# Kernel tuning notes

Hardware: AMD Instinct MI355X
Metric: run time of the kernel (lower is better)

Reference implementation:

```python
import jax, jax.numpy as jnp
import numpy as np

N_NODES = 100000
N_EDGES = 1600000
NEG_SLOPE = 0.2
EPS = 1e-16


def _gat_layer(x, src, dst, W, att_src, att_dst, bias, heads, out_ch):
    # x: [N, F_in]; src/dst: [E'] (self-loops already appended)
    n = x.shape[0]
    h = (x @ W).reshape(n, heads, out_ch)                      # [N, H, C]
    a_src = (h * att_src[None]).sum(-1)                        # [N, H]
    a_dst = (h * att_dst[None]).sum(-1)                        # [N, H]
    e = a_src[src] + a_dst[dst]                                # [E', H]
    e = jnp.where(e > 0, e, NEG_SLOPE * e)                     # leaky_relu
    # segment softmax over incoming edges of each dst node
    m = jax.ops.segment_max(e, dst, num_segments=n)            # [N, H]
    ex = jnp.exp(e - m[dst])                                   # [E', H]
    s = jax.ops.segment_sum(ex, dst, num_segments=n)           # [N, H]
    alpha = ex / (s[dst] + EPS)                                # [E', H]
    msg = h[src] * alpha[:, :, None]                           # [E', H, C]
    out = jax.ops.segment_sum(msg, dst, num_segments=n)        # [N, H, C]
    return out.reshape(n, heads * out_ch) + bias


def setup_inputs() -> dict:
    key = jax.random.key(0)
    ks = jax.random.split(key, 10)
    x = jax.random.normal(ks[0], (N_NODES, 165), dtype=jnp.float32)
    src = jax.random.randint(ks[1], (N_EDGES,), 0, N_NODES, dtype=jnp.int32)
    dst = jax.random.randint(ks[2], (N_EDGES,), 0, N_NODES, dtype=jnp.int32)
    glorot = lambda k, shp: jax.random.normal(k, shp, dtype=jnp.float32) * jnp.sqrt(2.0 / (shp[0] + shp[-1]))
    W1 = glorot(ks[3], (165, 256))
    att_src1 = glorot(ks[4], (4, 64))
    att_dst1 = glorot(ks[5], (4, 64))
    b1 = jnp.zeros((256,), dtype=jnp.float32)
    W2 = glorot(ks[6], (256, 2))
    att_src2 = glorot(ks[7], (1, 2))
    att_dst2 = glorot(ks[8], (1, 2))
    b2 = jnp.zeros((2,), dtype=jnp.float32)
    return {"x": x, "src": src, "dst": dst,
            "W1": W1, "att_src1": att_src1, "att_dst1": att_dst1, "b1": b1,
            "W2": W2, "att_src2": att_src2, "att_dst2": att_dst2, "b2": b2}


def reference(x, src, dst, W1, att_src1, att_dst1, b1, W2, att_src2, att_dst2, b2):
    n = x.shape[0]
    # PyG GATConv adds self-loops by default
    loops = jnp.arange(n, dtype=src.dtype)
    s = jnp.concatenate([src, loops])
    d = jnp.concatenate([dst, loops])
    h = _gat_layer(x, s, d, W1, att_src1, att_dst1, b1, heads=4, out_ch=64)
    h = jax.nn.relu(h)
    # F.dropout with training=False is identity (eval mode)
    out = _gat_layer(h, s, d, W2, att_src2, att_dst2, b2, heads=1, out_ch=2)
    return jax.nn.log_softmax(out, axis=1)
```

## Files before the change

### kernel.cpp

```cpp
#include <hip/hip_runtime.h>
#include <math.h>

#define NN 100000
#define NE 1600000
#define ET (NE + NN)
#define NEG 0.2f
#define KP 192
#define GEMM_BLKS (NN / 32)
#define SLOTS 64

typedef __attribute__((ext_vector_type(8))) short short8;
typedef __attribute__((ext_vector_type(4))) float floatx4;

__device__ __forceinline__ unsigned short f2bf(float f) {
    unsigned u = __float_as_uint(f);
    unsigned r = u + 0x7fffu + ((u >> 16) & 1u);
    return (unsigned short)(r >> 16);
}
__device__ __forceinline__ float bflo(unsigned x) { return __uint_as_float(x << 16); }
__device__ __forceinline__ float bfhi(unsigned x) { return __uint_as_float(x & 0xFFFF0000u); }

__global__ __launch_bounds__(256) void k_prep(const float* __restrict__ W,
                                              const float* __restrict__ x,
                                              unsigned short* __restrict__ Wt,
                                              int* __restrict__ deg,
                                              unsigned* __restrict__ xbf32) {
    const int gid = blockIdx.x * 256 + threadIdx.x;
    const int G = gridDim.x * 256;
    for (int idx = gid; idx < 256 * KP; idx += G) {
        const int n = idx / KP, k = idx - n * KP;
        Wt[idx] = (k < 165) ? f2bf(W[k * 256 + n]) : (unsigned short)0;
    }
    for (int i = gid; i < NN; i += G) deg[i] = 0;
    for (int p = gid; p < NN * (KP / 2); p += G) {
        const int n = p / (KP / 2), i = p - n * (KP / 2);
        const int k0 = 2 * i;
        const float v0 = (k0 < 165) ? x[(size_t)n * 165 + k0] : 0.0f;
        const float v1 = (k0 + 1 < 165) ? x[(size_t)n * 165 + k0 + 1] : 0.0f;
        xbf32[p] = (unsigned)f2bf(v0) | ((unsigned)f2bf(v1) << 16);
    }
}

__global__ __launch_bounds__(256) void k_histscat(const int* __restrict__ src,
                                                  const int* __restrict__ dst,
                                                  int* __restrict__ deg,
                                                  int* __restrict__ esrc) {
    const int e = blockIdx.x * 256 + threadIdx.x;
    if (e >= ET) return;
    int s, d;
    if (e < NE) { s = src[e]; d = dst[e]; } else { s = d = e - NE; }
    const int r = atomicAdd(&deg[d], 1);
    if (r < SLOTS) esrc[(d << 6) + r] = s;
}

__global__ __launch_bounds__(256) void k_gemm1(const unsigned short* __restrict__ xbf,
                                               const unsigned short* __restrict__ Wt,
                                               const float* __restrict__ att_s,
                                               const float* __restrict__ att_d,
                                               unsigned short* __restrict__ h1,
                                               float* __restrict__ a_src,
                                               float* __restrict__ a_dst) {
    __shared__ __align__(16) unsigned lds_p[32 * 132];
    const int t = threadIdx.x;
    const int n0 = blockIdx.x * 32;
    const int lane = t & 63, hd = t >> 6;
    const int r16 = lane & 15, quad = lane >> 4;
    floatx4 zero4 = {0.0f, 0.0f, 0.0f, 0.0f};
    floatx4 acc[2][4];
#pragma unroll
    for (int mm = 0; mm < 2; ++mm)
#pragma unroll
        for (int nn = 0; nn < 4; ++nn) acc[mm][nn] = zero4;

    const unsigned short* xr0 = xbf + (size_t)(n0 + r16) * KP;
    const unsigned short* xr1 = xbf + (size_t)(n0 + 16 + r16) * KP;
#pragma unroll
    for (int ks = 0; ks < 6; ++ks) {
        const int kb = ks * 32 + quad * 8;
        short8 a0 = *(const short8*)(xr0 + kb);
        short8 a1 = *(const short8*)(xr1 + kb);
        short8 bf[4];
#pragma unroll
        for (int nn = 0; nn < 4; ++nn)
            bf[nn] = *(const short8*)(Wt + (size_t)(hd * 64 + nn * 16 + r16) * KP + kb);
#pragma unroll
        for (int nn = 0; nn < 4; ++nn) {
            acc[0][nn] = __builtin_amdgcn_mfma_f32_16x16x32_bf16(a0, bf[nn], acc[0][nn], 0, 0, 0);
            acc[1][nn] = __builtin_amdgcn_mfma_f32_16x16x32_bf16(a1, bf[nn], acc[1][nn], 0, 0, 0);
        }
    }

    float asw[4], adw[4];
#pragma unroll
    for (int nn = 0; nn < 4; ++nn) {
        asw[nn] = att_s[hd * 64 + nn * 16 + r16];
        adw[nn] = att_d[hd * 64 + nn * 16 + r16];
    }
#pragma unroll
    for (int mm = 0; mm < 2; ++mm)
#pragma unroll
        for (int r = 0; r < 4; ++r) {
            float ps = acc[mm][0][r] * asw[0] + acc[mm][1][r] * asw[1] +
                       acc[mm][2][r] * asw[2] + acc[mm][3][r] * asw[3];
            float pd = acc[mm][0][r] * adw[0] + acc[mm][1][r] * adw[1] +
                       acc[mm][2][r] * adw[2] + acc[mm][3][r] * adw[3];
            ps += __shfl_xor(ps, 1); ps += __shfl_xor(ps, 2);
            ps += __shfl_xor(ps, 4); ps += __shfl_xor(ps, 8);
            pd += __shfl_xor(pd, 1); pd += __shfl_xor(pd, 2);
            pd += __shfl_xor(pd, 4); pd += __shfl_xor(pd, 8);
            if (r16 == 0) {
                const int node = n0 + mm * 16 + quad * 4 + r;
                a_src[node * 4 + hd] = ps;
                a_dst[node * 4 + hd] = pd;
            }
        }

#pragma unroll
    for (int mm = 0; mm < 2; ++mm)
#pragma unroll
        for (int nn = 0; nn < 4; ++nn)
#pragma unroll
            for (int r = 0; r < 4; ++r) {
                const float v = acc[mm][nn][r];
                const float o = __shfl_xor(v, 1);
                if ((lane & 1) == 0) {
                    const unsigned pk = (unsigned)f2bf(v) | ((unsigned)f2bf(o) << 16);
                    lds_p[(mm * 16 + quad * 4 + r) * 132 + hd * 32 + nn * 8 + (r16 >> 1)] = pk;
                }
            }
    __syncthreads();
    {
        const int row = t & 31, seg = t >> 5;
        const unsigned* p = &lds_p[row * 132 + seg * 16];
        uint4 d0 = *(const uint4*)(p);
        uint4 d1 = *(const uint4*)(p + 4);
        uint4 d2 = *(const uint4*)(p + 8);
        uint4 d3 = *(const uint4*)(p + 12);
        unsigned short* hp = h1 + (size_t)(n0 + row) * 256 + seg * 32;
        *(uint4*)(hp) = d0;
        *(uint4*)(hp + 8) = d1;
        *(uint4*)(hp + 16) = d2;
        *(uint4*)(hp + 24) = d3;
    }
}

__global__ __launch_bounds__(256) void k_l1agg(const unsigned short* __restrict__ h1,
                                               const float* __restrict__ a_src,
                                               const float* __restrict__ a_dst,
                                               const int* __restrict__ deg,
                                               const int* __restrict__ esrc,
                                               const float* __restrict__ b1,
                                               const float* __restrict__ W2,
                                               const float* __restrict__ att_s2,
                                               const float* __restrict__ att_d2,
                                               float4* __restrict__ node2) {
    const int t = threadIdx.x;
    const int n = blockIdx.x * 4 + (t >> 6);
    const int l = t & 63;
    const int q = l >> 4;
    const int sl = l & 15;
    const int head = sl >> 2;
    const int c0 = sl * 16;
    const int el = l >> 2;
    const int hl = l & 3;
    const int dg = deg[n];
    const int ebase = n << 6;
    const float4 ad4 = *(const float4*)&a_dst[n * 4];
    const float adh = (hl == 0) ? ad4.x : (hl == 1) ? ad4.y : (hl == 2) ? ad4.z : ad4.w;

    float ssum = 0.0f;
    float acc[16];
#pragma unroll
    for (int c = 0; c < 16; ++c) acc[c] = 0.0f;

    for (int base = 0; base < dg; base += 16) {
        const int cnt = dg - base;
        const int iters = (cnt < 16) ? cnt : 16;
        int sA = 0; float pA = 0.0f;
        if (el < cnt) {
            sA = esrc[ebase + base + el];
            const float a = a_src[sA * 4 + hl] + adh;
            const float e = (a > 0.0f) ? a : NEG * a;
            pA = __expf(e);
        }
#pragma unroll
        for (int jb = 0; jb < 16; jb += 4) {
            const int j = jb + q;
            const int s = __shfl(sA, j << 2);
            const float p = __shfl(pA, (j << 2) | head);
            if (j < iters) {
                ssum += p;
                const unsigned ho = ((unsigned)s << 8) + c0;
                const uint4 hv0 = *(const uint4*)(h1 + ho);
                const uint4 hv1 = *(const uint4*)(h1 + ho + 8);
                acc[0]  += p * bflo(hv0.x); acc[1]  += p * bfhi(hv0.x);
                acc[2]  += p * bflo(hv0.y); acc[3]  += p * bfhi(hv0.y);
                acc[4]  += p * bflo(hv0.z); acc[5]  += p * bfhi(hv0.z);
                acc[6]  += p * bflo(hv0.w); acc[7]  += p * bfhi(hv0.w);
                acc[8]  += p * bflo(hv1.x); acc[9]  += p * bfhi(hv1.x);
                acc[10] += p * bflo(hv1.y); acc[11] += p * bfhi(hv1.y);
                acc[12] += p * bflo(hv1.z); acc[13] += p * bfhi(hv1.z);
                acc[14] += p * bflo(hv1.w); acc[15] += p * bfhi(hv1.w);
            }
        }
    }
    ssum += __shfl_xor(ssum, 16); ssum += __shfl_xor(ssum, 32);
#pragma unroll
    for (int c = 0; c < 16; ++c) {
        acc[c] += __shfl_xor(acc[c], 16);
        acc[c] += __shfl_xor(acc[c], 32);
    }
    const float inv = 1.0f / ssum;
    float p0 = 0.0f, p1 = 0.0f;
#pragma unroll
    for (int c = 0; c < 16; ++c) {
        const float v = fmaxf(acc[c] * inv + b1[c0 + c], 0.0f);
        p0 += v * W2[(c0 + c) * 2 + 0];
        p1 += v * W2[(c0 + c) * 2 + 1];
    }
    if (q) { p0 = 0.0f; p1 = 0.0f; }
#pragma unroll
    for (int off = 32; off; off >>= 1) {
        p0 += __shfl_down(p0, off);
        p1 += __shfl_down(p1, off);
    }
    if (l == 0) {
        const float as2v = p0 * att_s2[0] + p1 * att_s2[1];
        const float ad2v = p0 * att_d2[0] + p1 * att_d2[1];
        node2[n] = make_float4(p0, p1, as2v, ad2v);
    }
}

__global__ __launch_bounds__(256) void k_l2agg(const float4* __restrict__ node2,
                                               const int* __restrict__ deg,
                                               const int* __restrict__ esrc,
                                               const float* __restrict__ b2,
                                               float* __restrict__ out) {
    const int t = threadIdx.x;
    const int l = t & 63;
    const int g = l >> 4;
    const int i = l & 15;
    const int n = blockIdx.x * 16 + (t >> 6) * 4 + g;
    const int dg = deg[n];
    const int ebase = n << 6;
    const float adst = node2[n].w;
    float ssum = 0.0f, a0 = 0.0f, a1 = 0.0f;
    for (int idx = i; idx < dg; idx += 16) {
        const int s = esrc[ebase + idx];
        const float4 r = node2[s];
        const float a = r.z + adst;
        const float e = (a > 0.0f) ? a : NEG * a;
        const float p = __expf(e);
        ssum += p; a0 += p * r.x; a1 += p * r.y;
    }
#pragma unroll
    for (int off = 8; off; off >>= 1) {
        ssum += __shfl_xor(ssum, off);
        a0 += __shfl_xor(a0, off);
        a1 += __shfl_xor(a1, off);
    }
    if (i == 0) {
        const float inv = 1.0f / ssum;
        const float z0 = a0 * inv + b2[0];
        const float z1 = a1 * inv + b2[1];
        const float mz = fmaxf(z0, z1);
        const float lse = mz + __logf(__expf(z0 - mz) + __expf(z1 - mz));
        out[n * 2 + 0] = z0 - lse;
        out[n * 2 + 1] = z1 - lse;
    }
}

extern "C" void kernel_launch(void* const* d_in, const int* in_sizes, int n_in,
                              void* d_out, int out_size, void* d_ws, size_t ws_size,
                              hipStream_t stream) {
    const float* x    = (const float*)d_in[0];
    const int*   src  = (const int*)d_in[1];
    const int*   dst  = (const int*)d_in[2];
    const float* W1   = (const float*)d_in[3];
    const float* as1w = (const float*)d_in[4];
    const float* ad1w = (const float*)d_in[5];
    const float* b1   = (const float*)d_in[6];
    const float* W2   = (const float*)d_in[7];
    const float* as2w = (const float*)d_in[8];
    const float* ad2w = (const float*)d_in[9];
    const float* b2   = (const float*)d_in[10];
    float* out = (float*)d_out;

    char* w = (char*)d_ws;
    unsigned short* h1  = (unsigned short*)w; w += (size_t)NN * 256 * 2;
    unsigned short* Wt  = (unsigned short*)w; w += (size_t)256 * KP * 2;
    unsigned short* xbf = (unsigned short*)w; w += (size_t)NN * KP * 2;
    float* a_src = (float*)w; w += (size_t)NN * 4 * 4;
    float* a_dst = (float*)w; w += (size_t)NN * 4 * 4;
    float4* node2 = (float4*)w; w += (size_t)NN * 4 * 4;
    int* deg     = (int*)w;   w += (size_t)NN * 4;
    int* esrc    = (int*)w;   w += (size_t)NN * SLOTS * 4;

    k_prep<<<2048, 256, 0, stream>>>(W1, x, Wt, deg, (unsigned*)xbf);
    k_histscat<<<(ET + 255) / 256, 256, 0, stream>>>(src, dst, deg, esrc);
    k_gemm1<<<GEMM_BLKS, 256, 0, stream>>>(xbf, Wt, as1w, ad1w, h1, a_src, a_dst);
    k_l1agg<<<NN / 4, 256, 0, stream>>>(h1, a_src, a_dst, deg, esrc, b1, W2, as2w, ad2w, node2);
    k_l2agg<<<NN / 16, 256, 0, stream>>>(node2, deg, esrc, b2, out);
}
```

Baseline: 459.5 us.

## Pre-bucket edges by destination range before scattering into per-node slot lists

Replaces the single atomic histogram-and-scatter kernel with a two-pass scheme. First, edges are grouped in shared memory into 25 coarse destination buckets and written contiguously to a global staging buffer. A second kernel then performs the per-node atomic slot assignment bucket by bucket, which is meant to improve locality of the deg/esrc atomics and writes. Self-loops are now initialized directly in the prep kernel. The cost is an extra kernel launch, an extra round trip through a 16 MB staging buffer, and a fixed bucket capacity that could overflow for skewed destination distributions.

```diff
diff --git a/kernel.cpp b/kernel.cpp
--- a/kernel.cpp
+++ b/kernel.cpp
@@ -9,6 +9,12 @@
 #define GEMM_BLKS (NN / 32)
 #define SLOTS 64
 
+#define NB 25
+#define BCAP 80000
+#define EPB 2048
+#define NBLK_BKT ((NE + EPB - 1) / EPB)
+#define TOTSLOT (NB * BCAP)
+
 typedef __attribute__((ext_vector_type(8))) short short8;
 typedef __attribute__((ext_vector_type(4))) float floatx4;
 
@@ -24,6 +30,8 @@
                                               const float* __restrict__ x,
                                               unsigned short* __restrict__ Wt,
                                               int* __restrict__ deg,
+                                              int* __restrict__ esrc,
+                                              int* __restrict__ gcur,
                                               unsigned* __restrict__ xbf32) {
     const int gid = blockIdx.x * 256 + threadIdx.x;
     const int G = gridDim.x * 256;
@@ -31,7 +39,8 @@
         const int n = idx / KP, k = idx - n * KP;
         Wt[idx] = (k < 165) ? f2bf(W[k * 256 + n]) : (unsigned short)0;
     }
-    for (int i = gid; i < NN; i += G) deg[i] = 0;
+    for (int i = gid; i < NN; i += G) { deg[i] = 1; esrc[i << 6] = i; }
+    for (int i = gid; i < NB; i += G) gcur[i] = i * BCAP;
     for (int p = gid; p < NN * (KP / 2); p += G) {
         const int n = p / (KP / 2), i = p - n * (KP / 2);
         const int k0 = 2 * i;
@@ -41,16 +50,65 @@
     }
 }
 
-__global__ __launch_bounds__(256) void k_histscat(const int* __restrict__ src,
-                                                  const int* __restrict__ dst,
-                                                  int* __restrict__ deg,
-                                                  int* __restrict__ esrc) {
-    const int e = blockIdx.x * 256 + threadIdx.x;
-    if (e >= ET) return;
-    int s, d;
-    if (e < NE) { s = src[e]; d = dst[e]; } else { s = d = e - NE; }
-    const int r = atomicAdd(&deg[d], 1);
-    if (r < SLOTS) esrc[(d << 6) + r] = s;
+__global__ __launch_bounds__(256) void k_bucket(const int* __restrict__ src,
+                                                const int* __restrict__ dst,
+                                                int* __restrict__ gcur,
+                                                unsigned long long* __restrict__ gstage) {
+    __shared__ int h[NB], lo[NB], base[NB], cur[NB];
+    __shared__ unsigned long long stage[EPB];
+    const int t = threadIdx.x;
+    const int e0 = blockIdx.x * EPB;
+    const int vc = (NE - e0 < EPB) ? (NE - e0) : EPB;
+    if (t < NB) h[t] = 0;
+    __syncthreads();
+    int dd[8], ss[8];
+#pragma unroll
+    for (int r = 0; r < 8; ++r) {
+        const int i = t + r * 256;
+        if (i < vc) {
+            dd[r] = dst[e0 + i];
+            ss[r] = src[e0 + i];
+            atomicAdd(&h[dd[r] >> 12], 1);
+        }
+    }
+    __syncthreads();
+    if (t == 0) { int run = 0; for (int b = 0; b < NB; ++b) { lo[b] = run; run += h[b]; } }
+    if (t < NB) cur[t] = 0;
+    __syncthreads();
+    if (t < NB && h[t] > 0) base[t] = atomicAdd(&gcur[t], h[t]);
+#pragma unroll
+    for (int r = 0; r < 8; ++r) {
+        const int i = t + r * 256;
+        if (i < vc) {
+            const int b = dd[r] >> 12;
+            const int p = atomicAdd(&cur[b], 1);
+            stage[lo[b] + p] = ((unsigned long long)(unsigned)dd[r] << 32) | (unsigned)ss[r];
+        }
+    }
+    __syncthreads();
+    for (int i = t; i < vc; i += 256) {
+        const unsigned long long rec = stage[i];
+        const int b = (int)(rec >> 44);
+        gstage[(size_t)base[b] + (i - lo[b])] = rec;
+    }
+}
+
+__global__ __launch_bounds__(256) void k_scatter(const unsigned long long* __restrict__ gstage,
+                                                 const int* __restrict__ gcur,
+                                                 int* __restrict__ deg,
+                                                 int* __restrict__ esrc) {
+    const int i = blockIdx.x * 256 + threadIdx.x;
+    if (i >= TOTSLOT) return;
+    const int p = i / BCAP;
+    const int within = i - p * BCAP;
+    const int cnt = gcur[p] - p * BCAP;
+    if (within < cnt) {
+        const unsigned long long rec = gstage[i];
+        const int d = (int)(rec >> 32);
+        const int s = (int)(unsigned)rec;
+        const int r = atomicAdd(&deg[d], 1);
+        if (r < SLOTS) esrc[(d << 6) + r] = s;
+    }
 }
 
 __global__ __launch_bounds__(256) void k_gemm1(const unsigned short* __restrict__ xbf,
@@ -295,9 +353,12 @@
     float4* node2 = (float4*)w; w += (size_t)NN * 4 * 4;
     int* deg     = (int*)w;   w += (size_t)NN * 4;
     int* esrc    = (int*)w;   w += (size_t)NN * SLOTS * 4;
-
-    k_prep<<<2048, 256, 0, stream>>>(W1, x, Wt, deg, (unsigned*)xbf);
-    k_histscat<<<(ET + 255) / 256, 256, 0, stream>>>(src, dst, deg, esrc);
+    unsigned long long* gstage = (unsigned long long*)w; w += (size_t)TOTSLOT * 8;
+    int* gcur    = (int*)w;   w += (size_t)NB * 4;
+
+    k_prep<<<2048, 256, 0, stream>>>(W1, x, Wt, deg, esrc, gcur, (unsigned*)xbf);
+    k_bucket<<<NBLK_BKT, 256, 0, stream>>>(src, dst, gcur, gstage);
+    k_scatter<<<(TOTSLOT + 255) / 256, 256, 0, stream>>>(gstage, gcur, deg, esrc);
     k_gemm1<<<GEMM_BLKS, 256, 0, stream>>>(xbf, Wt, as1w, ad1w, h1, a_src, a_dst);
     k_l1agg<<<NN / 4, 256, 0, stream>>>(h1, a_src, a_dst, deg, esrc, b1, W2, as2w, ad2w, node2);
     k_l2agg<<<NN / 16, 256, 0, stream>>>(node2, deg, esrc, b2, out);
```

Result: no change. 456.3 us (-0.7%).
